# Kernel tuning notes

Hardware: AMD Instinct MI355X
Metric: run time of the kernel (lower is better)

## Reference

```python
import jax, jax.numpy as jnp
import numpy as np
import math

B, N, EPG = 128, 512, 8192            # graphs, nodes/graph, edges/graph
E = B * EPG
DIN, H, DOUT = 128, 128, 10
RATIO = 0.8
K1 = math.ceil(RATIO * N)             # 410 nodes/graph after pool 1
K2 = math.ceil(RATIO * K1)            # 328 nodes/graph after pool 2
EPS = 1e-5


def setup_inputs() -> dict:
    key = jax.random.key(0)
    ks = jax.random.split(key, 16)
    x = jax.random.normal(ks[0], (B * N, DIN), jnp.float32)
    gid = jnp.repeat(jnp.arange(B, dtype=jnp.int32), EPG)
    src = jax.random.randint(ks[1], (E,), 0, N, dtype=jnp.int32) + gid * N
    dst = jax.random.randint(ks[2], (E,), 0, N, dtype=jnp.int32) + gid * N
    edge_index = jnp.stack([src, dst])

    def w(k, shape, fan_in):
        return jax.random.uniform(k, shape, jnp.float32, -1.0, 1.0) / np.sqrt(fan_in).astype(np.float32)

    return {
        "x": x, "edge_index": edge_index,
        "conv1_W": w(ks[3], (DIN, H), DIN), "conv1_b": jnp.zeros((H,), jnp.float32),
        "conv2_W": w(ks[4], (H, H), H),     "conv2_b": jnp.zeros((H,), jnp.float32),
        "score1_W": w(ks[5], (H, 1), H),    "score1_b": jnp.zeros((1,), jnp.float32),
        "score2_W": w(ks[6], (H, 1), H),    "score2_b": jnp.zeros((1,), jnp.float32),
        "bn1_g": jnp.ones((H,), jnp.float32), "bn1_b": jnp.zeros((H,), jnp.float32),
        "bn1_m": 0.1 * jax.random.normal(ks[7], (H,), jnp.float32),
        "bn1_v": jax.random.uniform(ks[8], (H,), jnp.float32, 0.5, 1.5),
        "bn2_g": jnp.ones((H,), jnp.float32), "bn2_b": jnp.zeros((H,), jnp.float32),
        "bn2_m": 0.1 * jax.random.normal(ks[9], (H,), jnp.float32),
        "bn2_v": jax.random.uniform(ks[10], (H,), jnp.float32, 0.5, 1.5),
        "lin0_W": w(ks[11], (DOUT, DIN), DIN), "lin0_b": jnp.zeros((DOUT,), jnp.float32),
        "lin1_W": w(ks[12], (DOUT, H), H),     "lin1_b": jnp.zeros((DOUT,), jnp.float32),
        "lin2_W": w(ks[13], (DOUT, H), H),     "lin2_b": jnp.zeros((DOUT,), jnp.float32),
    }


def gcn(h_in, src, dst, emask, W, b, n):
    # PyG GCNConv: self-loops + symmetric normalization D^-1/2 (A+I) D^-1/2 (XW) + b
    deg = jnp.ones((n,), h_in.dtype).at[dst].add(emask)      # self-loop counts as 1
    dinv = jax.lax.rsqrt(deg)
    coef = (dinv[src] * dinv[dst] * emask)[:, None]          # masked-out edges -> 0
    h = h_in @ W
    agg = jnp.zeros_like(h).at[dst].add(h[src] * coef)
    return agg + h * (dinv * dinv)[:, None] + b              # self-loop message + bias


def sag_pool(x, score, src, dst, emask, n_per, k):
    # topk per graph (equal-sized graphs -> static shapes), x <- x[perm]*tanh(score[perm])
    idx = jax.lax.top_k(score.reshape(B, n_per), k)[1]                      # [B,k]
    perm = (idx.astype(jnp.int32) + (jnp.arange(B, dtype=jnp.int32) * n_per)[:, None]).reshape(-1)
    xn = x[perm] * jnp.tanh(score[perm])[:, None]
    # filter_adj: remap surviving nodes, mask edges touching dropped nodes
    remap = jnp.full((B * n_per,), -1, jnp.int32).at[perm].set(jnp.arange(B * k, dtype=jnp.int32))
    s2, d2 = remap[src], remap[dst]
    em2 = emask * (s2 >= 0).astype(emask.dtype) * (d2 >= 0).astype(emask.dtype)
    return xn, jnp.maximum(s2, 0), jnp.maximum(d2, 0), em2


def bn_relu(x, g, b, m, v):
    # eval-mode BatchNorm1d followed by ReLU
    return jax.nn.relu(g * (x - m) * jax.lax.rsqrt(v + EPS) + b)


def reference(x, edge_index, conv1_W, conv1_b, conv2_W, conv2_b,
              score1_W, score1_b, score2_W, score2_b,
              bn1_g, bn1_b, bn1_m, bn1_v, bn2_g, bn2_b, bn2_m, bn2_v,
              lin0_W, lin0_b, lin1_W, lin1_b, lin2_W, lin2_b):
    src, dst = edge_index[0], edge_index[1]
    emask = jnp.ones((E,), x.dtype)
    hidden = [(x, N)]
    # layer 0: GCNConv -> SAGPool -> BN -> ReLU
    h = gcn(x, src, dst, emask, conv1_W, conv1_b, B * N)
    s = gcn(h, src, dst, emask, score1_W, score1_b, B * N)[:, 0]
    h, src, dst, emask = sag_pool(h, s, src, dst, emask, N, K1)
    h = bn_relu(h, bn1_g, bn1_b, bn1_m, bn1_v)
    hidden.append((h, K1))
    # layer 1
    h = gcn(h, src, dst, emask, conv2_W, conv2_b, B * K1)
    s = gcn(h, src, dst, emask, score2_W, score2_b, B * K1)[:, 0]
    h, src, dst, emask = sag_pool(h, s, src, dst, emask, K1, K2)
    h = bn_relu(h, bn2_g, bn2_b, bn2_m, bn2_v)
    hidden.append((h, K2))
    # jumping-knowledge readout: global_add_pool each rep, per-layer linear, sum (dropout eval = id)
    lins = [(lin0_W, lin0_b), (lin1_W, lin1_b), (lin2_W, lin2_b)]
    out = jnp.zeros((B, DOUT), x.dtype)
    for (hh, n_per), (W, bb) in zip(hidden, lins):
        pooled = hh.reshape(B, n_per, -1).sum(axis=1)   # global_add_pool (segment sum)
        out = out + pooled @ W.T + bb
    return out
```

## Files before the change

### kernel.cpp

```cpp
#include <hip/hip_runtime.h>

#define Bg   128
#define NPG  512
#define EPGc 8192
#define Etot (Bg*EPGc)
#define DOUTc 10
#define K1c  410
#define K2c  328
#define N0c  (Bg*NPG)
#define N1c  (Bg*K1c)
#define N2c  (Bg*K2c)
#define EPSc 1e-5f

static __global__ __launch_bounds__(512) void k_prep0(const int* __restrict__ src,
                                                      const int* __restrict__ dst,
                                                      float* __restrict__ dinv,
                                                      int* __restrict__ rp,
                                                      int2* __restrict__ e2,
                                                      float* __restrict__ pooled) {
  __shared__ int   cnt[NPG];
  __shared__ float sdv[NPG];
  __shared__ int   srp[NPG];
  __shared__ int   sbuf[512];
  int g = blockIdx.x, tid = threadIdx.x;
  if (tid < 128) {
    pooled[g * 128 + tid] = 0.f;
    pooled[Bg * 128 + g * 128 + tid] = 0.f;
    pooled[2 * Bg * 128 + g * 128 + tid] = 0.f;
  }
  cnt[tid] = 0;
  __syncthreads();
  const int* sp = src + (size_t)g * EPGc;
  const int* dp = dst + (size_t)g * EPGc;
  for (int e = tid; e < EPGc; e += 512) atomicAdd(&cnt[dp[e] - g * NPG], 1);
  __syncthreads();
  int c = cnt[tid];
  float dv = 1.0f / sqrtf(1.0f + (float)c);
  sdv[tid] = dv;
  dinv[g * NPG + tid] = dv;
  sbuf[tid] = c;
  __syncthreads();
  for (int off = 1; off < 512; off <<= 1) {
    int t = (tid >= off) ? sbuf[tid - off] : 0;
    __syncthreads();
    sbuf[tid] += t;
    __syncthreads();
  }
  srp[tid] = sbuf[tid] - c;
  rp[g * (NPG + 1) + tid] = sbuf[tid] - c;
  if (tid == 511) rp[g * (NPG + 1) + NPG] = sbuf[511];
  cnt[tid] = 0;
  __syncthreads();
  for (int e = tid; e < EPGc; e += 512) {
    int s = sp[e], d = dp[e];
    int dl = d - g * NPG;
    int pos = srp[dl] + atomicAdd(&cnt[dl], 1);
    e2[(size_t)g * EPGc + pos] =
        make_int2(s, __float_as_int(sdv[s - g * NPG] * sdv[dl]));
  }
}

static __global__ __launch_bounds__(512) void k_gemm2(const float* __restrict__ X,
                                                      const float* __restrict__ W,
                                                      float* __restrict__ Y, int M) {
  __shared__ float ws[128 * 128];
  __shared__ float xs[128 * 132];
  int tid = threadIdx.x;
  for (int i = tid; i < 4096; i += 512) ((float4*)ws)[i] = ((const float4*)W)[i];
  int row0 = blockIdx.x * 128;
  for (int i = tid; i < 4096; i += 512) {
    int r = i >> 5, kq = i & 31;
    float4 v = ((const float4*)X)[(size_t)(row0 + r) * 32 + kq];
    *(float4*)&xs[r * 132 + kq * 4] = v;
  }
  __syncthreads();
  int tx = tid & 15, ty = tid >> 4;
  float acc[4][8];
#pragma unroll
  for (int i = 0; i < 4; ++i)
#pragma unroll
    for (int j = 0; j < 8; ++j) acc[i][j] = 0.f;
  for (int k = 0; k < 128; k += 4) {
    float4 xr[4];
#pragma unroll
    for (int i = 0; i < 4; ++i) xr[i] = *(const float4*)&xs[(ty * 4 + i) * 132 + k];
    const float* xf = (const float*)xr;
#pragma unroll
    for (int kk = 0; kk < 4; ++kk) {
      float4 wa = *(const float4*)&ws[(k + kk) * 128 + tx * 4];
      float4 wb = *(const float4*)&ws[(k + kk) * 128 + 64 + tx * 4];
#pragma unroll
      for (int i = 0; i < 4; ++i) {
        float xv = xf[i * 4 + kk];
        acc[i][0] += xv * wa.x; acc[i][1] += xv * wa.y;
        acc[i][2] += xv * wa.z; acc[i][3] += xv * wa.w;
        acc[i][4] += xv * wb.x; acc[i][5] += xv * wb.y;
        acc[i][6] += xv * wb.z; acc[i][7] += xv * wb.w;
      }
    }
  }
#pragma unroll
  for (int i = 0; i < 4; ++i) {
    int row = row0 + ty * 4 + i;
    float4 o1 = make_float4(acc[i][0], acc[i][1], acc[i][2], acc[i][3]);
    float4 o2 = make_float4(acc[i][4], acc[i][5], acc[i][6], acc[i][7]);
    ((float4*)Y)[(size_t)row * 32 + tx] = o1;
    ((float4*)Y)[(size_t)row * 32 + 16 + tx] = o2;
  }
}

template <int NPER, int RG>
static __global__ __launch_bounds__(256) void k_agg3(const float* __restrict__ h0,
                                                     const float* __restrict__ dinv,
                                                     const float* __restrict__ bias,
                                                     const int* __restrict__ rp,
                                                     const int2* __restrict__ e2,
                                                     const float* __restrict__ sw,
                                                     float* __restrict__ h1,
                                                     float* __restrict__ spre) {
  int tid = threadIdx.x;
  int hw = tid >> 5, l = tid & 31;
  int b = blockIdx.x;
  int xcd = b & 7, slot = b >> 3;
  int g = xcd * 16 + (slot & 15);
  int rowgrp = slot >> 4;
  int li = rowgrp * 8 + hw;
  if (li >= NPER) return;
  int j = g * NPER + li;
  const int* rpg = rp + g * (NPER + 1);
  int start = rpg[li], end = rpg[li + 1];
  const int2* ep = e2 + (size_t)g * EPGc;
  float di = dinv[j];
  float sc = di * di;
  float4 acc = *(const float4*)&h0[(size_t)j * 128 + l * 4];
  float4 bb = ((const float4*)bias)[l];
  acc.x = acc.x * sc + bb.x; acc.y = acc.y * sc + bb.y;
  acc.z = acc.z * sc + bb.z; acc.w = acc.w * sc + bb.w;
  int e = start;
  for (; e + 4 <= end; e += 4) {
    int2 p0 = ep[e], p1 = ep[e + 1], p2 = ep[e + 2], p3 = ep[e + 3];
    float4 v0 = *(const float4*)&h0[(size_t)p0.x * 128 + l * 4];
    float4 v1 = *(const float4*)&h0[(size_t)p1.x * 128 + l * 4];
    float4 v2 = *(const float4*)&h0[(size_t)p2.x * 128 + l * 4];
    float4 v3 = *(const float4*)&h0[(size_t)p3.x * 128 + l * 4];
    float c0 = __int_as_float(p0.y), c1 = __int_as_float(p1.y);
    float c2 = __int_as_float(p2.y), c3 = __int_as_float(p3.y);
    acc.x += v0.x * c0 + v1.x * c1 + v2.x * c2 + v3.x * c3;
    acc.y += v0.y * c0 + v1.y * c1 + v2.y * c2 + v3.y * c3;
    acc.z += v0.z * c0 + v1.z * c1 + v2.z * c2 + v3.z * c3;
    acc.w += v0.w * c0 + v1.w * c1 + v2.w * c2 + v3.w * c3;
  }
  for (; e < end; ++e) {
    int2 pp = ep[e];
    float c = __int_as_float(pp.y);
    float4 v = *(const float4*)&h0[(size_t)pp.x * 128 + l * 4];
    acc.x += v.x * c; acc.y += v.y * c; acc.z += v.z * c; acc.w += v.w * c;
  }
  ((float4*)&h1[(size_t)j * 128])[l] = acc;
  float4 w4 = ((const float4*)sw)[l];
  float pr = acc.x * w4.x + acc.y * w4.y + acc.z * w4.z + acc.w * w4.w;
#pragma unroll
  for (int off = 16; off; off >>= 1) pr += __shfl_xor(pr, off, 64);
  if (l == 0) spre[j] = pr;
}

template <int NPER>
static __global__ void k_score2(const float* __restrict__ spre, const float* __restrict__ dinv,
                                const float* __restrict__ bptr, const int* __restrict__ rp,
                                const int2* __restrict__ e2, float* __restrict__ s, int n) {
  int j = blockIdx.x * 256 + threadIdx.x;
  if (j >= n) return;
  int g = j / NPER, li = j - g * NPER;
  const int* rpg = rp + g * (NPER + 1);
  int start = rpg[li], end = rpg[li + 1];
  const int2* ep = e2 + (size_t)g * EPGc;
  float di = dinv[j];
  float acc = spre[j] * di * di + bptr[0];
  int e = start;
  for (; e + 4 <= end; e += 4) {
    int2 p0 = ep[e], p1 = ep[e + 1], p2 = ep[e + 2], p3 = ep[e + 3];
    float a0 = spre[p0.x], a1 = spre[p1.x], a2 = spre[p2.x], a3 = spre[p3.x];
    acc += a0 * __int_as_float(p0.y) + a1 * __int_as_float(p1.y) +
           a2 * __int_as_float(p2.y) + a3 * __int_as_float(p3.y);
  }
  for (; e < end; ++e) { int2 pp = ep[e]; acc += spre[pp.x] * __int_as_float(pp.y); }
  s[j] = acc;
}

template <int NPER, int K>
static __global__ __launch_bounds__(512) void k_repool(const float* __restrict__ sv,
                                                       const int* __restrict__ src,
                                                       const int* __restrict__ dst,
                                                       int* __restrict__ perm,
                                                       float* __restrict__ dinv,
                                                       int* __restrict__ rp,
                                                       int2* __restrict__ e2) {
  __shared__ float sc[512];
  __shared__ int   sidx[512];
  __shared__ short remap[NPER];
  __shared__ int   cnt[K];
  __shared__ float sdv[K];
  __shared__ int   srp[K];
  __shared__ int   sbuf[512];
  int g = blockIdx.x, tid = threadIdx.x;
  sc[tid] = (tid < NPER) ? sv[g * NPER + tid] : -3.402823466e38f;
  sidx[tid] = tid;
  if (tid < NPER) remap[tid] = -1;
  __syncthreads();
  for (int kk = 2; kk <= 512; kk <<= 1) {
    for (int j = kk >> 1; j > 0; j >>= 1) {
      int i = tid, p = i ^ j;
      if (p > i) {
        bool up = ((i & kk) == 0);
        float si = sc[i], sp2 = sc[p];
        if (up ? (si < sp2) : (si > sp2)) {
          sc[i] = sp2; sc[p] = si;
          int t = sidx[i]; sidx[i] = sidx[p]; sidx[p] = t;
        }
      }
      __syncthreads();
    }
  }
  if (tid < K) {
    perm[g * K + tid] = g * NPER + sidx[tid];
    remap[sidx[tid]] = (short)tid;
    cnt[tid] = 0;
  }
  __syncthreads();
  const int* sp = src + (size_t)g * EPGc;
  const int* dp = dst + (size_t)g * EPGc;
  for (int e = tid; e < EPGc; e += 512) {
    int s = remap[sp[e] - g * NPER];
    int d = remap[dp[e] - g * NPER];
    if (s >= 0 && d >= 0) atomicAdd(&cnt[d], 1);
  }
  __syncthreads();
  int c = (tid < K) ? cnt[tid] : 0;
  if (tid < K) {
    float dv = 1.0f / sqrtf(1.0f + (float)c);
    sdv[tid] = dv;
    dinv[g * K + tid] = dv;
  }
  sbuf[tid] = c;
  __syncthreads();
  for (int off = 1; off < 512; off <<= 1) {
    int t = (tid >= off) ? sbuf[tid - off] : 0;
    __syncthreads();
    sbuf[tid] += t;
    __syncthreads();
  }
  if (tid < K) { srp[tid] = sbuf[tid] - c; rp[g * (K + 1) + tid] = sbuf[tid] - c; cnt[tid] = 0; }
  if (tid == 511) rp[g * (K + 1) + K] = sbuf[511];
  __syncthreads();
  for (int e = tid; e < EPGc; e += 512) {
    int s = remap[sp[e] - g * NPER];
    int d = remap[dp[e] - g * NPER];
    if (s >= 0 && d >= 0) {
      int pos = srp[d] + atomicAdd(&cnt[d], 1);
      e2[(size_t)g * EPGc + pos] = make_int2(g * K + s, __float_as_int(sdv[s] * sdv[d]));
    }
  }
}

template <int NPER, int K>
static __global__ __launch_bounds__(256) void k_topk(const float* __restrict__ s,
                                                     int* __restrict__ perm) {
  __shared__ float sc[512];
  __shared__ int   idx[512];
  int g = blockIdx.x, tid = threadIdx.x;
  for (int i = tid; i < 512; i += 256) {
    if (i < NPER) { sc[i] = s[g * NPER + i]; idx[i] = i; }
    else          { sc[i] = -3.402823466e38f; idx[i] = 0; }
  }
  __syncthreads();
  for (int kk = 2; kk <= 512; kk <<= 1) {
    for (int j = kk >> 1; j > 0; j >>= 1) {
      for (int base = 0; base < 512; base += 256) {
        int i = base + tid;
        int p = i ^ j;
        if (p > i) {
          bool up = ((i & kk) == 0);
          float si = sc[i], sp = sc[p];
          if (up ? (si < sp) : (si > sp)) {
            sc[i] = sp; sc[p] = si;
            int t = idx[i]; idx[i] = idx[p]; idx[p] = t;
          }
        }
      }
      __syncthreads();
    }
  }
  for (int r = tid; r < K; r += 256) perm[g * K + r] = g * NPER + idx[r];
}

template <int NPER, int CH>
static __global__ __launch_bounds__(128) void k_poolbn(const float* __restrict__ h,
                                                       const float* __restrict__ s,
                                                       const int* __restrict__ perm,
                                                       const float* __restrict__ gg,
                                                       const float* __restrict__ bb,
                                                       const float* __restrict__ mm,
                                                       const float* __restrict__ vv,
                                                       float* __restrict__ xp,
                                                       float* __restrict__ pooledseg) {
  int g = blockIdx.x / CH, cidx = blockIdx.x - g * CH;
  int f = threadIdx.x;
  const int rows = (NPER + CH - 1) / CH;
  int r0 = cidx * rows, r1 = min(NPER, r0 + rows);
  float G = gg[f], Bb = bb[f], Mm = mm[f];
  float inv = 1.0f / sqrtf(vv[f] + EPSc);
  float acc = 0.f;
  for (int r = r0; r < r1; ++r) {
    int j = g * NPER + r;
    int old = perm[j];
    float t = tanhf(s[old]);
    float val = h[(size_t)old * 128 + f] * t;
    float o = G * (val - Mm) * inv + Bb;
    o = fmaxf(o, 0.0f);
    xp[(size_t)j * 128 + f] = o;
    acc += o;
  }
  atomicAdd(&pooledseg[g * 128 + f], acc);
}

static __global__ __launch_bounds__(128) void k_gsum2(const float* __restrict__ xp,
                                                      float* __restrict__ pooled,
                                                      int nper, int nchunk) {
  int g = blockIdx.x / nchunk, c = blockIdx.x - g * nchunk;
  int f = threadIdx.x;
  int rows = (nper + nchunk - 1) / nchunk;
  int r0 = c * rows;
  int r1 = min(nper, r0 + rows);
  if (r0 >= r1) return;
  float acc = 0.f;
  const float* p = xp + ((size_t)g * nper + r0) * 128 + f;
  for (int i = r0; i < r1; ++i, p += 128) acc += *p;
  atomicAdd(&pooled[g * 128 + f], acc);
}

static __global__ void k_final(const float* __restrict__ pooled,
                               const float* __restrict__ w0, const float* __restrict__ b0,
                               const float* __restrict__ w1, const float* __restrict__ b1,
                               const float* __restrict__ w2, const float* __restrict__ b2,
                               float* __restrict__ out) {
  int t = blockIdx.x * 256 + threadIdx.x;
  if (t >= Bg * DOUTc) return;
  int g = t / DOUTc, o = t - g * DOUTc;
  const float* p0 = pooled + g * 128;
  const float* p1 = pooled + Bg * 128 + g * 128;
  const float* p2 = pooled + 2 * Bg * 128 + g * 128;
  float acc = b0[o] + b1[o] + b2[o];
  for (int k = 0; k < 128; ++k)
    acc += p0[k] * w0[o * 128 + k] + p1[k] * w1[o * 128 + k] + p2[k] * w2[o * 128 + k];
  out[t] = acc;
}

extern "C" void kernel_launch(void* const* d_in, const int* in_sizes, int n_in,
                              void* d_out, int out_size, void* d_ws, size_t ws_size,
                              hipStream_t stream) {
  (void)in_sizes; (void)n_in; (void)out_size; (void)ws_size;
  const float* x    = (const float*)d_in[0];
  const int*   ei   = (const int*)d_in[1];
  const int*   src0 = ei;
  const int*   dst0 = ei + Etot;
  const float* c1W = (const float*)d_in[2];  const float* c1b = (const float*)d_in[3];
  const float* c2W = (const float*)d_in[4];  const float* c2b = (const float*)d_in[5];
  const float* s1W = (const float*)d_in[6];  const float* s1b = (const float*)d_in[7];
  const float* s2W = (const float*)d_in[8];  const float* s2b = (const float*)d_in[9];
  const float* bn1g = (const float*)d_in[10]; const float* bn1b = (const float*)d_in[11];
  const float* bn1m = (const float*)d_in[12]; const float* bn1v = (const float*)d_in[13];
  const float* bn2g = (const float*)d_in[14]; const float* bn2b = (const float*)d_in[15];
  const float* bn2m = (const float*)d_in[16]; const float* bn2v = (const float*)d_in[17];
  const float* l0W = (const float*)d_in[18]; const float* l0b = (const float*)d_in[19];
  const float* l1W = (const float*)d_in[20]; const float* l1b = (const float*)d_in[21];
  const float* l2W = (const float*)d_in[22]; const float* l2b = (const float*)d_in[23];
  float* out = (float*)d_out;

  char* p = (char*)d_ws;
  auto alloc = [&](size_t bytes) { char* q = p; p += (bytes + 255) & ~(size_t)255; return q; };
  float* h0    = (float*)alloc((size_t)N0c * 128 * 4);
  float* h1    = (float*)alloc((size_t)N0c * 128 * 4);
  float* xp1   = (float*)alloc((size_t)N1c * 128 * 4);
  float* xp2   = (float*)alloc((size_t)N2c * 128 * 4);
  float* dinv  = (float*)alloc((size_t)N0c * 4);
  int*   rp    = (int*)alloc((size_t)Bg * (NPG + 1) * 4);
  int2*  e2    = (int2*)alloc((size_t)Etot * 8);
  float* spre  = (float*)alloc((size_t)N0c * 4);
  float* sv    = (float*)alloc((size_t)N0c * 4);
  int*   perm  = (int*)alloc((size_t)N1c * 4);
  float* pooled= (float*)alloc((size_t)3 * Bg * 128 * 4);

  dim3 b256(256), b128(128), b512(512);

  k_prep0<<<Bg, b512, 0, stream>>>(src0, dst0, dinv, rp, e2, pooled);
  k_gemm2<<<N0c / 128, b512, 0, stream>>>(x, c1W, h0, N0c);
  k_agg3<NPG, 64><<<128 * 64, b256, 0, stream>>>(h0, dinv, c1b, rp, e2, s1W, h1, spre);
  k_score2<NPG><<<(N0c + 255) / 256, b256, 0, stream>>>(spre, dinv, s1b, rp, e2, sv, N0c);
  k_repool<NPG, K1c><<<Bg, b512, 0, stream>>>(sv, src0, dst0, perm, dinv, rp, e2);
  k_poolbn<K1c, 8><<<Bg * 8, b128, 0, stream>>>(h1, sv, perm, bn1g, bn1b, bn1m, bn1v,
                                                xp1, pooled + Bg * 128);

  float* g1 = h0;
  float* h2 = h1;
  k_gemm2<<<N1c / 128, b512, 0, stream>>>(xp1, c2W, g1, N1c);
  k_agg3<K1c, 52><<<128 * 52, b256, 0, stream>>>(g1, dinv, c2b, rp, e2, s2W, h2, spre);
  k_score2<K1c><<<(N1c + 255) / 256, b256, 0, stream>>>(spre, dinv, s2b, rp, e2, sv, N1c);
  k_topk<K1c, K2c><<<Bg, b256, 0, stream>>>(sv, perm);
  k_poolbn<K2c, 8><<<Bg * 8, b128, 0, stream>>>(h2, sv, perm, bn2g, bn2b, bn2m, bn2v,
                                                xp2, pooled + 2 * Bg * 128);

  k_gsum2<<<Bg * 16, b128, 0, stream>>>(x, pooled, NPG, 16);
  k_final<<<(Bg * DOUTc + 255) / 256, b256, 0, stream>>>(pooled, l0W, l0b, l1W, l1b, l2W, l2b, out);
}
```

Baseline: 394.6 us.

## Fuse score, top-k, pooling and BN into per-graph kernels

Score aggregation, bitonic top-k, edge re-indexing and the pool/BN/ReLU readout are merged into one per-graph kernel for layer 1 (k_repool1) and one for layer 2 (k_pool2). The raw-input global sum moves into k_prep0, and the second-layer pooled features are no longer written to memory. This drops several launches, the perm/sv/xp2 round trips and the atomics. The aggregation loop also gains an 8-wide unroll to keep more gathers in flight. The trade-off is that the heavy pool/BN traffic now runs on only 128 blocks, which may underuse the GPU compared with the earlier 1024-block kernels.

New measurement: 416.8 us. +5.6%, slower.

```diff
diff --git a/kernel.cpp b/kernel.cpp
--- a/kernel.cpp
+++ b/kernel.cpp
@@ -14,22 +14,37 @@
 
 static __global__ __launch_bounds__(512) void k_prep0(const int* __restrict__ src,
                                                       const int* __restrict__ dst,
+                                                      const float* __restrict__ x,
                                                       float* __restrict__ dinv,
                                                       int* __restrict__ rp,
                                                       int2* __restrict__ e2,
-                                                      float* __restrict__ pooled) {
-  __shared__ int   cnt[NPG];
-  __shared__ float sdv[NPG];
-  __shared__ int   srp[NPG];
-  __shared__ int   sbuf[512];
+                                                      float* __restrict__ pooled0) {
+  __shared__ int    cnt[NPG];
+  __shared__ float  sdv[NPG];
+  __shared__ int    srp[NPG];
+  __shared__ int    sbuf[512];
+  __shared__ float4 xred[512];
   int g = blockIdx.x, tid = threadIdx.x;
-  if (tid < 128) {
-    pooled[g * 128 + tid] = 0.f;
-    pooled[Bg * 128 + g * 128 + tid] = 0.f;
-    pooled[2 * Bg * 128 + g * 128 + tid] = 0.f;
-  }
   cnt[tid] = 0;
-  __syncthreads();
+  {
+    int c4 = tid & 31, rq = tid >> 5;
+    float4 a = make_float4(0.f, 0.f, 0.f, 0.f);
+    const float4* xp = (const float4*)(x + (size_t)g * NPG * 128);
+    for (int r = rq; r < NPG; r += 16) {
+      float4 v = xp[r * 32 + c4];
+      a.x += v.x; a.y += v.y; a.z += v.z; a.w += v.w;
+    }
+    xred[tid] = a;
+  }
+  __syncthreads();
+  if (tid < 32) {
+    float4 a = make_float4(0.f, 0.f, 0.f, 0.f);
+    for (int q = 0; q < 16; ++q) {
+      float4 v = xred[q * 32 + tid];
+      a.x += v.x; a.y += v.y; a.z += v.z; a.w += v.w;
+    }
+    ((float4*)&pooled0[g * 128])[tid] = a;
+  }
   const int* sp = src + (size_t)g * EPGc;
   const int* dp = dst + (size_t)g * EPGc;
   for (int e = tid; e < EPGc; e += 512) atomicAdd(&cnt[dp[e] - g * NPG], 1);
@@ -137,6 +152,20 @@
   acc.x = acc.x * sc + bb.x; acc.y = acc.y * sc + bb.y;
   acc.z = acc.z * sc + bb.z; acc.w = acc.w * sc + bb.w;
   int e = start;
+  for (; e + 8 <= end; e += 8) {
+    int2 p[8];
+#pragma unroll
+    for (int q = 0; q < 8; ++q) p[q] = ep[e + q];
+    float4 v[8];
+#pragma unroll
+    for (int q = 0; q < 8; ++q) v[q] = *(const float4*)&h0[(size_t)p[q].x * 128 + l * 4];
+#pragma unroll
+    for (int q = 0; q < 8; ++q) {
+      float c = __int_as_float(p[q].y);
+      acc.x += v[q].x * c; acc.y += v[q].y * c;
+      acc.z += v[q].z * c; acc.w += v[q].w * c;
+    }
+  }
   for (; e + 4 <= end; e += 4) {
     int2 p0 = ep[e], p1 = ep[e + 1], p2 = ep[e + 2], p3 = ep[e + 3];
     float4 v0 = *(const float4*)&h0[(size_t)p0.x * 128 + l * 4];
@@ -164,48 +193,53 @@
   if (l == 0) spre[j] = pr;
 }
 
-template <int NPER>
-static __global__ void k_score2(const float* __restrict__ spre, const float* __restrict__ dinv,
-                                const float* __restrict__ bptr, const int* __restrict__ rp,
-                                const int2* __restrict__ e2, float* __restrict__ s, int n) {
-  int j = blockIdx.x * 256 + threadIdx.x;
-  if (j >= n) return;
-  int g = j / NPER, li = j - g * NPER;
-  const int* rpg = rp + g * (NPER + 1);
-  int start = rpg[li], end = rpg[li + 1];
-  const int2* ep = e2 + (size_t)g * EPGc;
-  float di = dinv[j];
-  float acc = spre[j] * di * di + bptr[0];
-  int e = start;
-  for (; e + 4 <= end; e += 4) {
-    int2 p0 = ep[e], p1 = ep[e + 1], p2 = ep[e + 2], p3 = ep[e + 3];
-    float a0 = spre[p0.x], a1 = spre[p1.x], a2 = spre[p2.x], a3 = spre[p3.x];
-    acc += a0 * __int_as_float(p0.y) + a1 * __int_as_float(p1.y) +
-           a2 * __int_as_float(p2.y) + a3 * __int_as_float(p3.y);
-  }
-  for (; e < end; ++e) { int2 pp = ep[e]; acc += spre[pp.x] * __int_as_float(pp.y); }
-  s[j] = acc;
-}
-
-template <int NPER, int K>
-static __global__ __launch_bounds__(512) void k_repool(const float* __restrict__ sv,
-                                                       const int* __restrict__ src,
-                                                       const int* __restrict__ dst,
-                                                       int* __restrict__ perm,
-                                                       float* __restrict__ dinv,
-                                                       int* __restrict__ rp,
-                                                       int2* __restrict__ e2) {
+static __global__ __launch_bounds__(512) void k_repool1(const float* __restrict__ spre,
+                                                        const float* __restrict__ dinv,
+                                                        const float* __restrict__ sb,
+                                                        const int* __restrict__ rp,
+                                                        int2* __restrict__ e2,
+                                                        const int* __restrict__ src,
+                                                        const int* __restrict__ dst,
+                                                        const float* __restrict__ h1,
+                                                        const float* __restrict__ gg,
+                                                        const float* __restrict__ bbn,
+                                                        const float* __restrict__ mm,
+                                                        const float* __restrict__ vv,
+                                                        float* __restrict__ xp1,
+                                                        float* __restrict__ dinv2,
+                                                        int* __restrict__ rp2,
+                                                        float* __restrict__ pooled1) {
+  __shared__ float ss[NPG];
   __shared__ float sc[512];
   __shared__ int   sidx[512];
-  __shared__ short remap[NPER];
-  __shared__ int   cnt[K];
-  __shared__ float sdv[K];
-  __shared__ int   srp[K];
+  __shared__ short rmp[NPG];
+  __shared__ int   cnt[K1c];
+  __shared__ float sdv[K1c];
+  __shared__ int   srp[K1c];
   __shared__ int   sbuf[512];
+  __shared__ float pbuf[4 * 128];
   int g = blockIdx.x, tid = threadIdx.x;
-  sc[tid] = (tid < NPER) ? sv[g * NPER + tid] : -3.402823466e38f;
-  sidx[tid] = tid;
-  if (tid < NPER) remap[tid] = -1;
+  ss[tid] = spre[g * NPG + tid];
+  rmp[tid] = -1;
+  __syncthreads();
+  {
+    const int* rpg = rp + g * (NPG + 1);
+    int st = rpg[tid], en = rpg[tid + 1];
+    const int2* ep = e2 + (size_t)g * EPGc;
+    float di = dinv[g * NPG + tid];
+    float acc = ss[tid] * di * di + sb[0];
+    int e = st;
+    for (; e + 4 <= en; e += 4) {
+      int2 p0 = ep[e], p1 = ep[e + 1], p2 = ep[e + 2], p3 = ep[e + 3];
+      acc += ss[p0.x - g * NPG] * __int_as_float(p0.y) +
+             ss[p1.x - g * NPG] * __int_as_float(p1.y) +
+             ss[p2.x - g * NPG] * __int_as_float(p2.y) +
+             ss[p3.x - g * NPG] * __int_as_float(p3.y);
+    }
+    for (; e < en; ++e) { int2 pp = ep[e]; acc += ss[pp.x - g * NPG] * __int_as_float(pp.y); }
+    sc[tid] = acc;
+    sidx[tid] = tid;
+  }
   __syncthreads();
   for (int kk = 2; kk <= 512; kk <<= 1) {
     for (int j = kk >> 1; j > 0; j >>= 1) {
@@ -221,25 +255,21 @@
       __syncthreads();
     }
   }
-  if (tid < K) {
-    perm[g * K + tid] = g * NPER + sidx[tid];
-    remap[sidx[tid]] = (short)tid;
-    cnt[tid] = 0;
-  }
+  if (tid < K1c) { rmp[sidx[tid]] = (short)tid; cnt[tid] = 0; }
   __syncthreads();
   const int* sp = src + (size_t)g * EPGc;
   const int* dp = dst + (size_t)g * EPGc;
   for (int e = tid; e < EPGc; e += 512) {
-    int s = remap[sp[e] - g * NPER];
-    int d = remap[dp[e] - g * NPER];
-    if (s >= 0 && d >= 0) atomicAdd(&cnt[d], 1);
-  }
-  __syncthreads();
-  int c = (tid < K) ? cnt[tid] : 0;
-  if (tid < K) {
+    int s = rmp[sp[e] - g * NPG];
+    int d = rmp[dp[e] - g * NPG];
+    if ((s | d) >= 0) atomicAdd(&cnt[d], 1);
+  }
+  __syncthreads();
+  int c = (tid < K1c) ? cnt[tid] : 0;
+  if (tid < K1c) {
     float dv = 1.0f / sqrtf(1.0f + (float)c);
     sdv[tid] = dv;
-    dinv[g * K + tid] = dv;
+    dinv2[g * K1c + tid] = dv;
   }
   sbuf[tid] = c;
   __syncthreads();
@@ -249,93 +279,103 @@
     sbuf[tid] += t;
     __syncthreads();
   }
-  if (tid < K) { srp[tid] = sbuf[tid] - c; rp[g * (K + 1) + tid] = sbuf[tid] - c; cnt[tid] = 0; }
-  if (tid == 511) rp[g * (K + 1) + K] = sbuf[511];
+  if (tid < K1c) { srp[tid] = sbuf[tid] - c; rp2[g * (K1c + 1) + tid] = sbuf[tid] - c; cnt[tid] = 0; }
+  if (tid == 511) rp2[g * (K1c + 1) + K1c] = sbuf[511];
   __syncthreads();
   for (int e = tid; e < EPGc; e += 512) {
-    int s = remap[sp[e] - g * NPER];
-    int d = remap[dp[e] - g * NPER];
-    if (s >= 0 && d >= 0) {
+    int s = rmp[sp[e] - g * NPG];
+    int d = rmp[dp[e] - g * NPG];
+    if ((s | d) >= 0) {
       int pos = srp[d] + atomicAdd(&cnt[d], 1);
-      e2[(size_t)g * EPGc + pos] = make_int2(g * K + s, __float_as_int(sdv[s] * sdv[d]));
-    }
-  }
-}
-
-template <int NPER, int K>
-static __global__ __launch_bounds__(256) void k_topk(const float* __restrict__ s,
-                                                     int* __restrict__ perm) {
+      e2[(size_t)g * EPGc + pos] = make_int2(g * K1c + s, __float_as_int(sdv[s] * sdv[d]));
+    }
+  }
+  int f = tid & 127, rsub = tid >> 7;
+  float G = gg[f], Bb = bbn[f], Mm = mm[f];
+  float inv = 1.0f / sqrtf(vv[f] + EPSc);
+  float acc = 0.f;
+  for (int r = rsub; r < K1c; r += 4) {
+    int old = g * NPG + sidx[r];
+    float t = tanhf(sc[r]);
+    float val = h1[(size_t)old * 128 + f] * t;
+    float o = fmaxf(G * (val - Mm) * inv + Bb, 0.f);
+    xp1[((size_t)g * K1c + r) * 128 + f] = o;
+    acc += o;
+  }
+  pbuf[rsub * 128 + f] = acc;
+  __syncthreads();
+  if (tid < 128)
+    pooled1[g * 128 + tid] = pbuf[tid] + pbuf[128 + tid] + pbuf[256 + tid] + pbuf[384 + tid];
+}
+
+static __global__ __launch_bounds__(512) void k_pool2(const float* __restrict__ spre,
+                                                      const float* __restrict__ dinv2,
+                                                      const float* __restrict__ sb,
+                                                      const int* __restrict__ rp2,
+                                                      const int2* __restrict__ e2,
+                                                      const float* __restrict__ h2,
+                                                      const float* __restrict__ gg,
+                                                      const float* __restrict__ bbn,
+                                                      const float* __restrict__ mm,
+                                                      const float* __restrict__ vv,
+                                                      float* __restrict__ pooled2) {
+  __shared__ float ss[K1c];
   __shared__ float sc[512];
-  __shared__ int   idx[512];
+  __shared__ int   sidx[512];
+  __shared__ float pbuf[4 * 128];
   int g = blockIdx.x, tid = threadIdx.x;
-  for (int i = tid; i < 512; i += 256) {
-    if (i < NPER) { sc[i] = s[g * NPER + i]; idx[i] = i; }
-    else          { sc[i] = -3.402823466e38f; idx[i] = 0; }
-  }
+  if (tid < K1c) ss[tid] = spre[g * K1c + tid];
+  __syncthreads();
+  if (tid < K1c) {
+    const int* rpg = rp2 + g * (K1c + 1);
+    int st = rpg[tid], en = rpg[tid + 1];
+    const int2* ep = e2 + (size_t)g * EPGc;
+    float di = dinv2[g * K1c + tid];
+    float acc = ss[tid] * di * di + sb[0];
+    int e = st;
+    for (; e + 4 <= en; e += 4) {
+      int2 p0 = ep[e], p1 = ep[e + 1], p2 = ep[e + 2], p3 = ep[e + 3];
+      acc += ss[p0.x - g * K1c] * __int_as_float(p0.y) +
+             ss[p1.x - g * K1c] * __int_as_float(p1.y) +
+             ss[p2.x - g * K1c] * __int_as_float(p2.y) +
+             ss[p3.x - g * K1c] * __int_as_float(p3.y);
+    }
+    for (; e < en; ++e) { int2 pp = ep[e]; acc += ss[pp.x - g * K1c] * __int_as_float(pp.y); }
+    sc[tid] = acc;
+  } else {
+    sc[tid] = -3.402823466e38f;
+  }
+  sidx[tid] = tid;
   __syncthreads();
   for (int kk = 2; kk <= 512; kk <<= 1) {
     for (int j = kk >> 1; j > 0; j >>= 1) {
-      for (int base = 0; base < 512; base += 256) {
-        int i = base + tid;
-        int p = i ^ j;
-        if (p > i) {
-          bool up = ((i & kk) == 0);
-          float si = sc[i], sp = sc[p];
-          if (up ? (si < sp) : (si > sp)) {
-            sc[i] = sp; sc[p] = si;
-            int t = idx[i]; idx[i] = idx[p]; idx[p] = t;
-          }
+      int i = tid, p = i ^ j;
+      if (p > i) {
+        bool up = ((i & kk) == 0);
+        float si = sc[i], sp2 = sc[p];
+        if (up ? (si < sp2) : (si > sp2)) {
+          sc[i] = sp2; sc[p] = si;
+          int t = sidx[i]; sidx[i] = sidx[p]; sidx[p] = t;
         }
       }
       __syncthreads();
     }
   }
-  for (int r = tid; r < K; r += 256) perm[g * K + r] = g * NPER + idx[r];
-}
-
-template <int NPER, int CH>
-static __global__ __launch_bounds__(128) void k_poolbn(const float* __restrict__ h,
-                                                       const float* __restrict__ s,
-                                                       const int* __restrict__ perm,
-                                                       const float* __restrict__ gg,
-                                                       const float* __restrict__ bb,
-                                                       const float* __restrict__ mm,
-                                                       const float* __restrict__ vv,
-                                                       float* __restrict__ xp,
-                                                       float* __restrict__ pooledseg) {
-  int g = blockIdx.x / CH, cidx = blockIdx.x - g * CH;
-  int f = threadIdx.x;
-  const int rows = (NPER + CH - 1) / CH;
-  int r0 = cidx * rows, r1 = min(NPER, r0 + rows);
-  float G = gg[f], Bb = bb[f], Mm = mm[f];
+  int f = tid & 127, rsub = tid >> 7;
+  float G = gg[f], Bb = bbn[f], Mm = mm[f];
   float inv = 1.0f / sqrtf(vv[f] + EPSc);
   float acc = 0.f;
-  for (int r = r0; r < r1; ++r) {
-    int j = g * NPER + r;
-    int old = perm[j];
-    float t = tanhf(s[old]);
-    float val = h[(size_t)old * 128 + f] * t;
-    float o = G * (val - Mm) * inv + Bb;
-    o = fmaxf(o, 0.0f);
-    xp[(size_t)j * 128 + f] = o;
+  for (int r = rsub; r < K2c; r += 4) {
+    int old = g * K1c + sidx[r];
+    float t = tanhf(sc[r]);
+    float val = h2[(size_t)old * 128 + f] * t;
+    float o = fmaxf(G * (val - Mm) * inv + Bb, 0.f);
     acc += o;
   }
-  atomicAdd(&pooledseg[g * 128 + f], acc);
-}
-
-static __global__ __launch_bounds__(128) void k_gsum2(const float* __restrict__ xp,
-                                                      float* __restrict__ pooled,
-                                                      int nper, int nchunk) {
-  int g = blockIdx.x / nchunk, c = blockIdx.x - g * nchunk;
-  int f = threadIdx.x;
-  int rows = (nper + nchunk - 1) / nchunk;
-  int r0 = c * rows;
-  int r1 = min(nper, r0 + rows);
-  if (r0 >= r1) return;
-  float acc = 0.f;
-  const float* p = xp + ((size_t)g * nper + r0) * 128 + f;
-  for (int i = r0; i < r1; ++i, p += 128) acc += *p;
-  atomicAdd(&pooled[g * 128 + f], acc);
+  pbuf[rsub * 128 + f] = acc;
+  __syncthreads();
+  if (tid < 128)
+    pooled2[g * 128 + tid] = pbuf[tid] + pbuf[128 + tid] + pbuf[256 + tid] + pbuf[384 + tid];
 }
 
 static __global__ void k_final(const float* __restrict__ pooled,
@@ -381,34 +421,29 @@
   float* h0    = (float*)alloc((size_t)N0c * 128 * 4);
   float* h1    = (float*)alloc((size_t)N0c * 128 * 4);
   float* xp1   = (float*)alloc((size_t)N1c * 128 * 4);
-  float* xp2   = (float*)alloc((size_t)N2c * 128 * 4);
   float* dinv  = (float*)alloc((size_t)N0c * 4);
+  float* dinv2 = (float*)alloc((size_t)N1c * 4);
   int*   rp    = (int*)alloc((size_t)Bg * (NPG + 1) * 4);
+  int*   rp2   = (int*)alloc((size_t)Bg * (K1c + 1) * 4);
   int2*  e2    = (int2*)alloc((size_t)Etot * 8);
   float* spre  = (float*)alloc((size_t)N0c * 4);
-  float* sv    = (float*)alloc((size_t)N0c * 4);
-  int*   perm  = (int*)alloc((size_t)N1c * 4);
   float* pooled= (float*)alloc((size_t)3 * Bg * 128 * 4);
 
-  dim3 b256(256), b128(128), b512(512);
-
-  k_prep0<<<Bg, b512, 0, stream>>>(src0, dst0, dinv, rp, e2, pooled);
+  dim3 b256(256), b512(512);
+
+  k_prep0<<<Bg, b512, 0, stream>>>(src0, dst0, x, dinv, rp, e2, pooled);
   k_gemm2<<<N0c / 128, b512, 0, stream>>>(x, c1W, h0, N0c);
   k_agg3<NPG, 64><<<128 * 64, b256, 0, stream>>>(h0, dinv, c1b, rp, e2, s1W, h1, spre);
-  k_score2<NPG><<<(N0c + 255) / 256, b256, 0, stream>>>(spre, dinv, s1b, rp, e2, sv, N0c);
-  k_repool<NPG, K1c><<<Bg, b512, 0, stream>>>(sv, src0, dst0, perm, dinv, rp, e2);
-  k_poolbn<K1c, 8><<<Bg * 8, b128, 0, stream>>>(h1, sv, perm, bn1g, bn1b, bn1m, bn1v,
-                                                xp1, pooled + Bg * 128);
+  k_repool1<<<Bg, b512, 0, stream>>>(spre, dinv, s1b, rp, e2, src0, dst0, h1,
+                                     bn1g, bn1b, bn1m, bn1v, xp1, dinv2, rp2,
+                                     pooled + Bg * 128);
 
   float* g1 = h0;
   float* h2 = h1;
   k_gemm2<<<N1c / 128, b512, 0, stream>>>(xp1, c2W, g1, N1c);
-  k_agg3<K1c, 52><<<128 * 52, b256, 0, stream>>>(g1, dinv, c2b, rp, e2, s2W, h2, spre);
-  k_score2<K1c><<<(N1c + 255) / 256, b256, 0, stream>>>(spre, dinv, s2b, rp, e2, sv, N1c);
-  k_topk<K1c, K2c><<<Bg, b256, 0, stream>>>(sv, perm);
-  k_poolbn<K2c, 8><<<Bg * 8, b128, 0, stream>>>(h2, sv, perm, bn2g, bn2b, bn2m, bn2v,
-                                                xp2, pooled + 2 * Bg * 128);
-
-  k_gsum2<<<Bg * 16, b128, 0, stream>>>(x, pooled, NPG, 16);
+  k_agg3<K1c, 52><<<128 * 52, b256, 0, stream>>>(g1, dinv2, c2b, rp2, e2, s2W, h2, spre);
+  k_pool2<<<Bg, b512, 0, stream>>>(spre, dinv2, s2b, rp2, e2, h2,
+                                   bn2g, bn2b, bn2m, bn2v, pooled + 2 * Bg * 128);
+
   k_final<<<(Bg * DOUTc + 255) / 256, b256, 0, stream>>>(pooled, l0W, l0b, l1W, l1b, l2W, l2b, out);
 }
```
